# Kernel optimization log

Measured on AMD Instinct MI355X. Metric: run time of the kernel, lower is better.

## Reference

```python
import jax, jax.numpy as jnp
import numpy as np

B, S, D, E, TOPK = 8, 4096, 1024, 64, 2
TEMP = 0.01


def setup_inputs() -> dict:
    key = jax.random.key(0)
    k_x, k_w1, k_b1, k_w2, k_b2 = jax.random.split(key, 5)
    x = jax.random.normal(k_x, (B, S, D), dtype=jnp.float32)
    # torch.nn.Linear default init ~ U(-1/sqrt(fan_in), 1/sqrt(fan_in)); scale ok for reference
    W1 = jax.random.normal(k_w1, (D, 2 * D), dtype=jnp.float32) * (1.0 / np.sqrt(D))
    b1 = jax.random.normal(k_b1, (2 * D,), dtype=jnp.float32) * 0.01
    W2 = jax.random.normal(k_w2, (2 * D, E), dtype=jnp.float32) * (1.0 / np.sqrt(2 * D))
    b2 = jax.random.normal(k_b2, (E,), dtype=jnp.float32) * 0.01
    return {"x": x, "W1": W1, "b1": b1, "W2": W2, "b2": b2}


def reference(x, W1, b1, W2, b2):
    # 2-layer MLP router: [B,S,D] -> [B,S,2D] -> [B,S,E]
    h = jax.nn.relu(jnp.einsum('bsd,df->bsf', x, W1) + b1)
    logits = jnp.einsum('bsf,fe->bse', h, W2) + b2
    # top-k over experts
    top_k_logits, indices = jax.lax.top_k(logits, TOPK)  # [B,S,K]
    # scatter top-k logits into a -inf-filled tensor: equivalent to masking,
    # since scattered values equal logits at those positions
    keep = jax.nn.one_hot(indices, E, dtype=bool).any(axis=-2)  # [B,S,E]
    sparse_logits = jnp.where(keep, logits, -jnp.inf)
    router_output = jax.nn.softmax(sparse_logits, axis=-1)
    ori_router_output = jax.nn.softmax(logits / TEMP, axis=-1)
    return (ori_router_output, router_output, indices)
```

## Files before the change

### kernel.cpp

```cpp
#include <hip/hip_runtime.h>
#include <math.h>
#include <stdint.h>

#define M_TOK 32768
#define D_IN  1024
#define F_HID 2048
#define E_EXP 64

#define O_ORI 0
#define O_RTR (M_TOK * E_EXP)
#define O_IDX (2 * M_TOK * E_EXP)

typedef _Float16 half8 __attribute__((ext_vector_type(8)));
typedef float    f32x4 __attribute__((ext_vector_type(4)));
typedef unsigned int uint32;
typedef uint32   u32x4 __attribute__((ext_vector_type(4)));

#define WS_XH  ((size_t)0)
#define WS_XL  (WS_XH  + (size_t)M_TOK * D_IN * 2)
#define WS_W1H (WS_XL  + (size_t)M_TOK * D_IN * 2)
#define WS_W1L (WS_W1H + (size_t)D_IN * F_HID * 2)
#define WS_W2H (WS_W1L + (size_t)D_IN * F_HID * 2)
#define WS_W2L (WS_W2H + (size_t)F_HID * E_EXP * 2)
#define WS_NEED (WS_W2L + (size_t)F_HID * E_EXP * 2)

__device__ __forceinline__ void split_sc(float v, float sc, unsigned short& h, unsigned short& l) {
    const _Float16 hh = (_Float16)v;
    const float hf = (float)hh;
    const _Float16 hs = (_Float16)(hf * sc);
    const _Float16 ls = (_Float16)((v - hf) * sc);
    h = __builtin_bit_cast(unsigned short, hs);
    l = __builtin_bit_cast(unsigned short, ls);
}


__global__ void split_x_k(const float* __restrict__ x,
                          unsigned short* __restrict__ xh, unsigned short* __restrict__ xl) {
    size_t i = ((size_t)blockIdx.x * 256 + threadIdx.x) * 4;
    const float4 v = *(const float4*)&x[i];
    ushort4 h, l;
    split_sc(v.x, 64.f, h.x, l.x); split_sc(v.y, 64.f, h.y, l.y);
    split_sc(v.z, 64.f, h.z, l.z); split_sc(v.w, 64.f, h.w, l.w);
    *(ushort4*)&xh[i] = h;
    *(ushort4*)&xl[i] = l;
}

__global__ void split_w1t_k(const float* __restrict__ W1,
                            unsigned short* __restrict__ wh, unsigned short* __restrict__ wl) {
    __shared__ float t[32][33];
    const int d0 = blockIdx.x * 32;
    const int f0 = blockIdx.y * 32;
    const int r  = threadIdx.x >> 3;
    const int c4 = (threadIdx.x & 7) * 4;
    const float4 v = *(const float4*)&W1[(size_t)(d0 + r) * F_HID + f0 + c4];
    t[r][c4 + 0] = v.x; t[r][c4 + 1] = v.y; t[r][c4 + 2] = v.z; t[r][c4 + 3] = v.w;
    __syncthreads();
    ushort4 h, l;
    split_sc(t[c4 + 0][r], 64.f, h.x, l.x);
    split_sc(t[c4 + 1][r], 64.f, h.y, l.y);
    split_sc(t[c4 + 2][r], 64.f, h.z, l.z);
    split_sc(t[c4 + 3][r], 64.f, h.w, l.w);
    *(ushort4*)&wh[(size_t)(f0 + r) * D_IN + d0 + c4] = h;
    *(ushort4*)&wl[(size_t)(f0 + r) * D_IN + d0 + c4] = l;
}

__global__ void split_w2f_k(const float* __restrict__ W2,
                            unsigned short* __restrict__ wh, unsigned short* __restrict__ wl) {
    const int s  = blockIdx.x;
    const int nt = threadIdx.x >> 6;
    const int l  = threadIdx.x & 63;
    const int fb = s * 32 + (l >> 4) * 8;
    const int e  = nt * 16 + (l & 15);
    unsigned short h[8], lo[8];
#pragma unroll
    for (int j = 0; j < 8; ++j)
        split_sc(W2[(size_t)(fb + j) * E_EXP + e], 16.f, h[j], lo[j]);
    const size_t base = ((size_t)(s * 4 + nt) * 64 + l) * 8;
    ((ushort4*)&wh[base])[0] = make_ushort4(h[0], h[1], h[2], h[3]);
    ((ushort4*)&wh[base])[1] = make_ushort4(h[4], h[5], h[6], h[7]);
    ((ushort4*)&wl[base])[0] = make_ushort4(lo[0], lo[1], lo[2], lo[3]);
    ((ushort4*)&wl[base])[1] = make_ushort4(lo[4], lo[5], lo[6], lo[7]);
}


__device__ __forceinline__ uint32 swz(uint32 o) { return o ^ (((o >> 7) & 7u) << 4); }

#define STAGE16(SRCP, DSTP) \
    __builtin_amdgcn_global_load_lds((const __attribute__((address_space(1))) void*)(SRCP), \
                                     (__attribute__((address_space(3))) void*)(DSTP), 16, 0, 0)


#define A_BUF(b)  ((b) * 16384)
#define B_BUF(b)  (49152 + (b) * 32768)

__launch_bounds__(512, 2)
__global__ void router_one(const unsigned short* __restrict__ xh, const unsigned short* __restrict__ xl,
                           const unsigned short* __restrict__ w1h, const unsigned short* __restrict__ w1l,
                           const unsigned short* __restrict__ w2fh, const unsigned short* __restrict__ w2fl,
                           const float* __restrict__ b1, const float* __restrict__ b2,
                           float* __restrict__ out)
{
    __shared__ __align__(16) unsigned char lds[147456];

    const int tid  = threadIdx.x;
    const int lane = tid & 63;
    const int w    = tid >> 6;
    const int c15  = lane & 15;
    const int g    = lane >> 4;
    const int wr   = w >> 2;
    const int wc   = w & 3;

    const size_t tok0 = (size_t)blockIdx.x * 128;

    uint32 arow, ahalf, brow[2], bhalf[2];
    {
        const uint32 sA = swz((uint32)(tid * 16));
        arow = sA >> 6; ahalf = (sA & 63u) >> 1;
#pragma unroll
        for (int j = 0; j < 2; ++j) {
            const uint32 sB = swz((uint32)(j * 8192 + w * 1024 + lane * 16));
            brow[j] = sB >> 6; bhalf[j] = (sB & 63u) >> 1;
        }
    }

    uint32 offA[4], offB[4];
#pragma unroll
    for (int m = 0; m < 4; ++m)
        offA[m] = swz((uint32)((wr * 64 + m * 16 + c15) * 64 + g * 16));
#pragma unroll
    for (int n = 0; n < 4; ++n)
        offB[n] = swz((uint32)((wc * 64 + n * 16 + c15) * 64 + g * 16));

    f32x4 acc2[4];
#pragma unroll
    for (int nt = 0; nt < 4; ++nt) acc2[nt] = (f32x4){0.f, 0.f, 0.f, 0.f};

#define STAGE_A(T, WB, F0) do {                                                      \
    const int d0_ = (T) * 32;                                                        \
    const size_t asrc = (tok0 + arow) * D_IN + (size_t)(d0_ + (int)ahalf);           \
    STAGE16(xh + asrc, lds + A_BUF(WB) + w * 1024);                                  \
    STAGE16(xl + asrc, lds + A_BUF(WB) + 8192 + w * 1024);                           \
} while (0)
#define STAGE_B(T, WB, F0, J) do {                                                   \
    const int d0_ = (T) * 32;                                                        \
    const size_t bsrc = ((size_t)(F0) + brow[J]) * D_IN + (size_t)(d0_ + (int)bhalf[J]); \
    STAGE16(w1h + bsrc, lds + B_BUF(WB) + (J) * 8192 + w * 1024);                    \
    STAGE16(w1l + bsrc, lds + B_BUF(WB) + 16384 + (J) * 8192 + w * 1024);            \
} while (0)

#pragma unroll 1
    for (int fc = 0; fc < F_HID; fc += 256) {
        f32x4 acc[4][4];
#pragma unroll
        for (int m = 0; m < 4; ++m)
#pragma unroll
            for (int n = 0; n < 4; ++n) acc[m][n] = (f32x4){0.f, 0.f, 0.f, 0.f};

        __syncthreads();
        STAGE_A(0, 0, fc); STAGE_B(0, 0, fc, 0); STAGE_B(0, 0, fc, 1);
        STAGE_A(1, 1, fc); STAGE_B(1, 1, fc, 0); STAGE_B(1, 1, fc, 1);

#pragma unroll 1
        for (int t = 0; t < 32; ++t) {
            if (t < 31) asm volatile("s_waitcnt vmcnt(6)" ::: "memory");
            else        asm volatile("s_waitcnt vmcnt(0)" ::: "memory");
            __builtin_amdgcn_s_barrier();
            const int rb = t % 3;
            const int wb = (t + 2) % 3;
            const bool do_stage = (t + 2 < 32);
            const unsigned char* Ab = lds + A_BUF(rb);
            const unsigned char* Bb = lds + B_BUF(rb);

            half8 a1f[4], a2f[4], b1f[4], b2f[4];

#pragma unroll
            for (int m = 0; m < 4; ++m) {
                a1f[m] = *(const half8*)(Ab + offA[m]);
                a2f[m] = *(const half8*)(Ab + 8192 + offA[m]);
            }
            b1f[0] = *(const half8*)(Bb + offB[0]);
            b2f[0] = *(const half8*)(Bb + 16384 + offB[0]);
            if (do_stage) STAGE_A(t + 2, wb, fc);
            __builtin_amdgcn_s_barrier();
            asm volatile("s_waitcnt lgkmcnt(0)" ::: "memory");
            __builtin_amdgcn_s_setprio(1);
#pragma unroll
            for (int m = 0; m < 4; ++m) {
                acc[m][0] = __builtin_amdgcn_mfma_f32_16x16x32_f16(a1f[m], b1f[0], acc[m][0], 0, 0, 0);
                acc[m][0] = __builtin_amdgcn_mfma_f32_16x16x32_f16(a1f[m], b2f[0], acc[m][0], 0, 0, 0);
                acc[m][0] = __builtin_amdgcn_mfma_f32_16x16x32_f16(a2f[m], b1f[0], acc[m][0], 0, 0, 0);
            }
            __builtin_amdgcn_s_setprio(0);
            __builtin_amdgcn_s_barrier();

            b1f[1] = *(const half8*)(Bb + offB[1]);
            b2f[1] = *(const half8*)(Bb + 16384 + offB[1]);
            if (do_stage) STAGE_B(t + 2, wb, fc, 0);
            __builtin_amdgcn_s_barrier();
            asm volatile("s_waitcnt lgkmcnt(0)" ::: "memory");
            __builtin_amdgcn_s_setprio(1);
#pragma unroll
            for (int m = 0; m < 4; ++m) {
                acc[m][1] = __builtin_amdgcn_mfma_f32_16x16x32_f16(a1f[m], b1f[1], acc[m][1], 0, 0, 0);
                acc[m][1] = __builtin_amdgcn_mfma_f32_16x16x32_f16(a1f[m], b2f[1], acc[m][1], 0, 0, 0);
                acc[m][1] = __builtin_amdgcn_mfma_f32_16x16x32_f16(a2f[m], b1f[1], acc[m][1], 0, 0, 0);
            }
            __builtin_amdgcn_s_setprio(0);
            __builtin_amdgcn_s_barrier();

            b1f[2] = *(const half8*)(Bb + offB[2]);
            b2f[2] = *(const half8*)(Bb + 16384 + offB[2]);
            if (do_stage) STAGE_B(t + 2, wb, fc, 1);
            __builtin_amdgcn_s_barrier();
            asm volatile("s_waitcnt lgkmcnt(0)" ::: "memory");
            __builtin_amdgcn_s_setprio(1);
#pragma unroll
            for (int m = 0; m < 4; ++m) {
                acc[m][2] = __builtin_amdgcn_mfma_f32_16x16x32_f16(a1f[m], b1f[2], acc[m][2], 0, 0, 0);
                acc[m][2] = __builtin_amdgcn_mfma_f32_16x16x32_f16(a1f[m], b2f[2], acc[m][2], 0, 0, 0);
                acc[m][2] = __builtin_amdgcn_mfma_f32_16x16x32_f16(a2f[m], b1f[2], acc[m][2], 0, 0, 0);
            }
            __builtin_amdgcn_s_setprio(0);
            __builtin_amdgcn_s_barrier();

            b1f[3] = *(const half8*)(Bb + offB[3]);
            b2f[3] = *(const half8*)(Bb + 16384 + offB[3]);
            __builtin_amdgcn_s_barrier();
            asm volatile("s_waitcnt lgkmcnt(0)" ::: "memory");
            __builtin_amdgcn_s_setprio(1);
#pragma unroll
            for (int m = 0; m < 4; ++m) {
                acc[m][3] = __builtin_amdgcn_mfma_f32_16x16x32_f16(a1f[m], b1f[3], acc[m][3], 0, 0, 0);
                acc[m][3] = __builtin_amdgcn_mfma_f32_16x16x32_f16(a1f[m], b2f[3], acc[m][3], 0, 0, 0);
                acc[m][3] = __builtin_amdgcn_mfma_f32_16x16x32_f16(a2f[m], b1f[3], acc[m][3], 0, 0, 0);
            }
            __builtin_amdgcn_s_setprio(0);
        }

        __syncthreads();
        {
            float bv[4];
#pragma unroll
            for (int n = 0; n < 4; ++n) bv[n] = b1[fc + wc * 64 + n * 16 + c15];
#pragma unroll
            for (int m = 0; m < 4; ++m)
#pragma unroll
                for (int n = 0; n < 4; ++n)
#pragma unroll
                    for (int r = 0; r < 4; ++r) {
                        float hv = acc[m][n][r] * (1.f / 4096.f) + bv[n];
                        hv = fmaxf(hv, 0.f);
                        const _Float16 hh = (_Float16)hv;
                        const float hf = (float)hh;
                        const _Float16 hsv = (_Float16)(hf * 16.f);
                        const _Float16 lsv = (_Float16)((hv - hf) * 16.f);
                        const uint32 pk = (uint32)__builtin_bit_cast(unsigned short, hsv)
                                        | ((uint32)__builtin_bit_cast(unsigned short, lsv) << 16);
                        const int tok = wr * 64 + m * 16 + g * 4 + r;
                        const int fl  = wc * 64 + n * 16 + c15;
                        *(uint32*)(lds + tok * 1024 + ((fl * 4) ^ ((tok & 15) << 4))) = pk;
                    }
        }
        __syncthreads();

        {
            const int tokA = w * 16 + c15;
#pragma unroll
            for (int s = 0; s < 8; ++s) {
                const int kf = s * 32 + g * 8;
                const int sg = (fc >> 5) + s;
                half8 bf1[4], bf2[4];
#pragma unroll
                for (int nt = 0; nt < 4; ++nt) {
                    const size_t base = ((size_t)(sg * 4 + nt) * 64 + lane) * 8;
                    bf1[nt] = *(const half8*)&w2fh[base];
                    bf2[nt] = *(const half8*)&w2fl[base];
                }
                const u32x4 q0 = *(const u32x4*)(lds + tokA * 1024 + (((kf    ) * 4) ^ (c15 << 4)));
                const u32x4 q1 = *(const u32x4*)(lds + tokA * 1024 + (((kf + 4) * 4) ^ (c15 << 4)));
                u32x4 hi4, lo4;
                hi4[0] = __builtin_amdgcn_perm(q0[1], q0[0], 0x05040100u);
                hi4[1] = __builtin_amdgcn_perm(q0[3], q0[2], 0x05040100u);
                hi4[2] = __builtin_amdgcn_perm(q1[1], q1[0], 0x05040100u);
                hi4[3] = __builtin_amdgcn_perm(q1[3], q1[2], 0x05040100u);
                lo4[0] = __builtin_amdgcn_perm(q0[1], q0[0], 0x07060302u);
                lo4[1] = __builtin_amdgcn_perm(q0[3], q0[2], 0x07060302u);
                lo4[2] = __builtin_amdgcn_perm(q1[1], q1[0], 0x07060302u);
                lo4[3] = __builtin_amdgcn_perm(q1[3], q1[2], 0x07060302u);
                const half8 a1 = __builtin_bit_cast(half8, hi4);
                const half8 a2 = __builtin_bit_cast(half8, lo4);
#pragma unroll
                for (int nt = 0; nt < 4; ++nt) {
                    acc2[nt] = __builtin_amdgcn_mfma_f32_16x16x32_f16(a1, bf1[nt], acc2[nt], 0, 0, 0);
                    acc2[nt] = __builtin_amdgcn_mfma_f32_16x16x32_f16(a1, bf2[nt], acc2[nt], 0, 0, 0);
                    acc2[nt] = __builtin_amdgcn_mfma_f32_16x16x32_f16(a2, bf1[nt], acc2[nt], 0, 0, 0);
                }
            }
        }
    }
#undef STAGE_A
#undef STAGE_B

    __syncthreads();
    float* ls = (float*)lds;
#pragma unroll
    for (int nt = 0; nt < 4; ++nt)
#pragma unroll
        for (int r = 0; r < 4; ++r) {
            const int tl = w * 16 + g * 4 + r;
            ls[tl * 68 + nt * 16 + c15] = acc2[nt][r] * (1.f / 256.f);
        }
    __syncthreads();

    const int e = lane;
    const float be = b2[e];
#pragma unroll 1
    for (int i = 0; i < 16; ++i) {
        const float l = ls[(w * 16 + i) * 68 + e] + be;

        float v = l; int idx = e;
#pragma unroll
        for (int m = 32; m >= 1; m >>= 1) {
            const float ov = __shfl_xor(v, m, 64);
            const int   oi = __shfl_xor(idx, m, 64);
            if (ov > v || (ov == v && oi < idx)) { v = ov; idx = oi; }
        }
        const float m1 = v; const int i1 = idx;

        v = (e == i1) ? -INFINITY : l; idx = e;
#pragma unroll
        for (int m = 32; m >= 1; m >>= 1) {
            const float ov = __shfl_xor(v, m, 64);
            const int   oi = __shfl_xor(idx, m, 64);
            if (ov > v || (ov == v && oi < idx)) { v = ov; idx = oi; }
        }
        const int i2 = idx;

        const float ex = expf((l - m1) * 100.0f);
        float s = ex;
#pragma unroll
        for (int m = 32; m >= 1; m >>= 1) s += __shfl_xor(s, m, 64);
        const float ori = ex / s;

        const float q = (e == i1 || e == i2) ? expf(l - m1) : 0.f;
        float s2 = q;
#pragma unroll
        for (int m = 32; m >= 1; m >>= 1) s2 += __shfl_xor(s2, m, 64);
        const float rtr = q / s2;

        const size_t tok = tok0 + (size_t)w * 16 + i;
        out[O_ORI + tok * E_EXP + e] = ori;
        out[O_RTR + tok * E_EXP + e] = rtr;
        if (e == 0) {
            out[O_IDX + tok * 2 + 0] = (float)i1;
            out[O_IDX + tok * 2 + 1] = (float)i2;
        }
    }
}


#define BT  64
#define NB  256

__launch_bounds__(256, 2)
__global__ void router_mfma(const unsigned short* __restrict__ xh, const unsigned short* __restrict__ xl,
                            const unsigned short* __restrict__ w1h, const unsigned short* __restrict__ w1l,
                            const unsigned short* __restrict__ w2fh, const unsigned short* __restrict__ w2fl,
                            const float* __restrict__ b1, const float* __restrict__ b2,
                            float* __restrict__ out)
{
    __shared__ __align__(16) unsigned char xs_h[BT * 64];
    __shared__ __align__(16) unsigned char xs_l[BT * 64];
    __shared__ __align__(16) unsigned char w1s_h[NB * 64];
    __shared__ __align__(16) unsigned char w1s_l[NB * 64];
    __shared__ __align__(16) unsigned char hsbuf[BT * 132 * 4];

    const int tid  = threadIdx.x;
    const int lane = tid & 63;
    const int w    = tid >> 6;
    const int c15  = lane & 15;
    const int g    = lane >> 4;
    const size_t tok0 = (size_t)blockIdx.x * BT;

    uint32* hs = (uint32*)hsbuf;
    float*  ls = (float*)hsbuf;

    f32x4 acc2h[4], acc2x[4];
#pragma unroll
    for (int nt = 0; nt < 4; ++nt) {
        acc2h[nt] = (f32x4){0.f, 0.f, 0.f, 0.f};
        acc2x[nt] = (f32x4){0.f, 0.f, 0.f, 0.f};
    }

    const uint32 kqb = (uint32)g * 16u;

    for (int fc = 0; fc < F_HID; fc += NB) {
        f32x4 ahh[4][4], axx[4][4];
#pragma unroll
        for (int mt = 0; mt < 4; ++mt)
#pragma unroll
            for (int nt = 0; nt < 4; ++nt) {
                ahh[mt][nt] = (f32x4){0.f, 0.f, 0.f, 0.f};
                axx[mt][nt] = (f32x4){0.f, 0.f, 0.f, 0.f};
            }

        for (int d0 = 0; d0 < D_IN; d0 += 32) {
            __syncthreads();
            {
                uint32 o = (uint32)w * 1024u + (uint32)lane * 16u;
                uint32 s = swz(o);
                uint32 r = s >> 6, hb = (s & 63u) >> 1;
                const unsigned short* sp;
                sp = xh + (tok0 + r) * D_IN + (size_t)(d0 + (int)hb);
                STAGE16(sp, xs_h + (size_t)w * 1024);
                sp = xl + (tok0 + r) * D_IN + (size_t)(d0 + (int)hb);
                STAGE16(sp, xs_l + (size_t)w * 1024);
#pragma unroll
                for (int q = 0; q < 4; ++q) {
                    const uint32 c_ = (uint32)(q * 4 + w);
                    uint32 o2 = c_ * 1024u + (uint32)lane * 16u;
                    uint32 s2 = swz(o2);
                    uint32 r2 = s2 >> 6, hb2 = (s2 & 63u) >> 1;
                    sp = w1h + ((size_t)(fc + (int)r2)) * D_IN + (size_t)(d0 + (int)hb2);
                    STAGE16(sp, w1s_h + (size_t)c_ * 1024);
                    sp = w1l + ((size_t)(fc + (int)r2)) * D_IN + (size_t)(d0 + (int)hb2);
                    STAGE16(sp, w1s_l + (size_t)c_ * 1024);
                }
            }
            __syncthreads();

            half8 ah[4], al[4], bh[4], bl[4];
#pragma unroll
            for (int mt = 0; mt < 4; ++mt) {
                const uint32 off = swz((uint32)(mt * 16 + c15) * 64u + kqb);
                ah[mt] = *(const half8*)(xs_h + off);
                al[mt] = *(const half8*)(xs_l + off);
            }
#pragma unroll
            for (int nt = 0; nt < 4; ++nt) {
                const uint32 row = (uint32)(w * 64 + nt * 16 + c15);
                const uint32 off = swz(row * 64u + kqb);
                bh[nt] = *(const half8*)(w1s_h + off);
                bl[nt] = *(const half8*)(w1s_l + off);
            }
#pragma unroll
            for (int mt = 0; mt < 4; ++mt)
#pragma unroll
                for (int nt = 0; nt < 4; ++nt) {
                    ahh[mt][nt] = __builtin_amdgcn_mfma_f32_16x16x32_f16(ah[mt], bh[nt], ahh[mt][nt], 0, 0, 0);
                    axx[mt][nt] = __builtin_amdgcn_mfma_f32_16x16x32_f16(ah[mt], bl[nt], axx[mt][nt], 0, 0, 0);
                    axx[mt][nt] = __builtin_amdgcn_mfma_f32_16x16x32_f16(al[mt], bh[nt], axx[mt][nt], 0, 0, 0);
                }
        }

        const int fl0 = (w & 1) * 64;
#pragma unroll
        for (int phase = 0; phase < 2; ++phase) {
            if ((w >> 1) == phase) {
#pragma unroll
                for (int nt = 0; nt < 4; ++nt) {
                    const float b1v = b1[fc + w * 64 + nt * 16 + c15];
#pragma unroll
                    for (int mt = 0; mt < 4; ++mt) {
#pragma unroll
                        for (int r = 0; r < 4; ++r) {
                            float hv = (ahh[mt][nt][r] + axx[mt][nt][r]) * (1.f / 4096.f) + b1v;
                            hv = fmaxf(hv, 0.f);
                            const _Float16 hhv0 = (_Float16)hv;
                            const float hf = (float)hhv0;
                            const _Float16 hhv = (_Float16)(hf * 16.f);
                            const _Float16 hlv = (_Float16)((hv - hf) * 16.f);
                            uint32 pk = (uint32)__builtin_bit_cast(unsigned short, hhv)
                                      | ((uint32)__builtin_bit_cast(unsigned short, hlv) << 16);
                            const int t = mt * 16 + g * 4 + r;
                            hs[t * 132 + fl0 + nt * 16 + c15] = pk;
                        }
                    }
                }
            }
            __syncthreads();
            const int tA = w * 16 + c15;
#pragma unroll
            for (int ktl = 0; ktl < 4; ++ktl) {
                const u32x4 q0 = *(const u32x4*)&hs[tA * 132 + ktl * 32 + g * 8];
                const u32x4 q1 = *(const u32x4*)&hs[tA * 132 + ktl * 32 + g * 8 + 4];
                u32x4 hi4, lo4;
                hi4[0] = __builtin_amdgcn_perm(q0[1], q0[0], 0x05040100u);
                hi4[1] = __builtin_amdgcn_perm(q0[3], q0[2], 0x05040100u);
                hi4[2] = __builtin_amdgcn_perm(q1[1], q1[0], 0x05040100u);
                hi4[3] = __builtin_amdgcn_perm(q1[3], q1[2], 0x05040100u);
                lo4[0] = __builtin_amdgcn_perm(q0[1], q0[0], 0x07060302u);
                lo4[1] = __builtin_amdgcn_perm(q0[3], q0[2], 0x07060302u);
                lo4[2] = __builtin_amdgcn_perm(q1[1], q1[0], 0x07060302u);
                lo4[3] = __builtin_amdgcn_perm(q1[3], q1[2], 0x07060302u);
                const half8 a_h = __builtin_bit_cast(half8, hi4);
                const half8 a_l = __builtin_bit_cast(half8, lo4);
                const int sg = (fc >> 5) + phase * 4 + ktl;
#pragma unroll
                for (int nt = 0; nt < 4; ++nt) {
                    const size_t base = ((size_t)(sg * 4 + nt) * 64 + lane) * 8;
                    const half8 b_h = *(const half8*)&w2fh[base];
                    const half8 b_l = *(const half8*)&w2fl[base];
                    acc2h[nt] = __builtin_amdgcn_mfma_f32_16x16x32_f16(a_h, b_h, acc2h[nt], 0, 0, 0);
                    acc2x[nt] = __builtin_amdgcn_mfma_f32_16x16x32_f16(a_h, b_l, acc2x[nt], 0, 0, 0);
                    acc2x[nt] = __builtin_amdgcn_mfma_f32_16x16x32_f16(a_l, b_h, acc2x[nt], 0, 0, 0);
                }
            }
            __syncthreads();
        }
    }

#pragma unroll
    for (int nt = 0; nt < 4; ++nt)
#pragma unroll
        for (int r = 0; r < 4; ++r) {
            const int t = w * 16 + g * 4 + r;
            ls[t * 68 + nt * 16 + c15] = (acc2h[nt][r] + acc2x[nt][r]) * (1.f / 256.f);
        }
    __syncthreads();

    const int e = lane;
    const float be = b2[e];
#pragma unroll 1
    for (int i = 0; i < 16; ++i) {
        const float l = ls[(w * 16 + i) * 68 + e] + be;

        float v = l; int idx = e;
#pragma unroll
        for (int m = 32; m >= 1; m >>= 1) {
            const float ov = __shfl_xor(v, m, 64);
            const int   oi = __shfl_xor(idx, m, 64);
            if (ov > v || (ov == v && oi < idx)) { v = ov; idx = oi; }
        }
        const float m1 = v; const int i1 = idx;

        v = (e == i1) ? -INFINITY : l; idx = e;
#pragma unroll
        for (int m = 32; m >= 1; m >>= 1) {
            const float ov = __shfl_xor(v, m, 64);
            const int   oi = __shfl_xor(idx, m, 64);
            if (ov > v || (ov == v && oi < idx)) { v = ov; idx = oi; }
        }
        const int i2 = idx;

        const float ex = expf((l - m1) * 100.0f);
        float s = ex;
#pragma unroll
        for (int m = 32; m >= 1; m >>= 1) s += __shfl_xor(s, m, 64);
        const float ori = ex / s;

        const float q = (e == i1 || e == i2) ? expf(l - m1) : 0.f;
        float s2 = q;
#pragma unroll
        for (int m = 32; m >= 1; m >>= 1) s2 += __shfl_xor(s2, m, 64);
        const float rtr = q / s2;

        const size_t tok = tok0 + (size_t)w * 16 + i;
        out[O_ORI + tok * E_EXP + e] = ori;
        out[O_RTR + tok * E_EXP + e] = rtr;
        if (e == 0) {
            out[O_IDX + tok * 2 + 0] = (float)i1;
            out[O_IDX + tok * 2 + 1] = (float)i2;
        }
    }
}


extern "C" void kernel_launch(void* const* d_in, const int* in_sizes, int n_in,
                              void* d_out, int out_size, void* d_ws, size_t ws_size,
                              hipStream_t stream) {
    const float* x  = (const float*)d_in[0];
    const float* W1 = (const float*)d_in[1];
    const float* b1 = (const float*)d_in[2];
    const float* W2 = (const float*)d_in[3];
    const float* b2 = (const float*)d_in[4];
    float* out = (float*)d_out;

    unsigned char* ws = (unsigned char*)d_ws;
    unsigned short* xh  = (unsigned short*)(ws + WS_XH);
    unsigned short* xl  = (unsigned short*)(ws + WS_XL);
    unsigned short* w1h = (unsigned short*)(ws + WS_W1H);
    unsigned short* w1l = (unsigned short*)(ws + WS_W1L);
    unsigned short* w2h = (unsigned short*)(ws + WS_W2H);
    unsigned short* w2l = (unsigned short*)(ws + WS_W2L);

    hipLaunchKernelGGL(split_x_k,  dim3(M_TOK * D_IN / 4 / 256), dim3(256), 0, stream, x, xh, xl);
    hipLaunchKernelGGL(split_w1t_k, dim3(D_IN / 32, F_HID / 32), dim3(256), 0, stream, W1, w1h, w1l);
    hipLaunchKernelGGL(split_w2f_k, dim3(F_HID / 32), dim3(256), 0, stream, W2, w2h, w2l);

    if (ws_size >= WS_NEED) {
        hipLaunchKernelGGL(router_one, dim3(M_TOK / 128), dim3(512), 0, stream,
                           xh, xl, w1h, w1l, w2h, w2l, b1, b2, out);
    } else {
        hipLaunchKernelGGL(router_mfma, dim3(M_TOK / BT), dim3(256), 0, stream,
                           xh, xl, w1h, w1l, w2h, w2l, b1, b2, out);
    }
}
```

Baseline: 498.8 us.

## Switch first GEMM to 32x32x16 MFMA tiles with deeper LDS swizzle

Replaces the 16x16x32 MFMA inner product of the first layer with 32x32x16 MFMA instructions, so each wave computes 2x2 tiles of 32x32 instead of 4x4 tiles of 16x16. LDS fragment reads are regrouped to fit the new operand layout, and the swizzle XORs in additional address bits to avoid bank conflicts under the new access pattern. The per-iteration phases drop from four to two, with both B stagings issued together. The epilogue index mapping is updated to the 32x32 accumulator layout. The larger MFMA should cut LDS traffic per flop and the number of barriers, at the cost of coarser interleaving between loads and compute.

```diff
diff --git a/kernel.cpp b/kernel.cpp
--- a/kernel.cpp
+++ b/kernel.cpp
@@ -12,7 +12,8 @@
 #define O_IDX (2 * M_TOK * E_EXP)
 
 typedef _Float16 half8 __attribute__((ext_vector_type(8)));
-typedef float    f32x4 __attribute__((ext_vector_type(4)));
+typedef float    f32x4  __attribute__((ext_vector_type(4)));
+typedef float    f32x16 __attribute__((ext_vector_type(16)));
 typedef unsigned int uint32;
 typedef uint32   u32x4 __attribute__((ext_vector_type(4)));
 
@@ -83,7 +84,9 @@
 }
 
 
-__device__ __forceinline__ uint32 swz(uint32 o) { return o ^ (((o >> 7) & 7u) << 4); }
+__device__ __forceinline__ uint32 swz(uint32 o) {
+    return o ^ (((((o >> 7) & 7u) ^ ((o >> 10) & 7u))) << 4);
+}
 
 #define STAGE16(SRCP, DSTP) \
     __builtin_amdgcn_global_load_lds((const __attribute__((address_space(1))) void*)(SRCP), \
@@ -107,6 +110,8 @@
     const int w    = tid >> 6;
     const int c15  = lane & 15;
     const int g    = lane >> 4;
+    const int c31  = lane & 31;
+    const int g32  = lane >> 5;
     const int wr   = w >> 2;
     const int wc   = w & 3;
 
@@ -123,19 +128,23 @@
         }
     }
 
-    uint32 offA[4], offB[4];
-#pragma unroll
-    for (int m = 0; m < 4; ++m)
-        offA[m] = swz((uint32)((wr * 64 + m * 16 + c15) * 64 + g * 16));
-#pragma unroll
-    for (int n = 0; n < 4; ++n)
-        offB[n] = swz((uint32)((wc * 64 + n * 16 + c15) * 64 + g * 16));
+    uint32 offA[2][2], offB[2][2];
+#pragma unroll
+    for (int mt = 0; mt < 2; ++mt)
+#pragma unroll
+        for (int ks = 0; ks < 2; ++ks)
+            offA[mt][ks] = swz((uint32)((wr * 64 + mt * 32 + c31) * 64 + ks * 32 + g32 * 16));
+#pragma unroll
+    for (int nt = 0; nt < 2; ++nt)
+#pragma unroll
+        for (int ks = 0; ks < 2; ++ks)
+            offB[nt][ks] = swz((uint32)((wc * 64 + nt * 32 + c31) * 64 + ks * 32 + g32 * 16));
 
     f32x4 acc2[4];
 #pragma unroll
     for (int nt = 0; nt < 4; ++nt) acc2[nt] = (f32x4){0.f, 0.f, 0.f, 0.f};
 
-#define STAGE_A(T, WB, F0) do {                                                      \
+#define STAGE_A(T, WB) do {                                                          \
     const int d0_ = (T) * 32;                                                        \
     const size_t asrc = (tok0 + arow) * D_IN + (size_t)(d0_ + (int)ahalf);           \
     STAGE16(xh + asrc, lds + A_BUF(WB) + w * 1024);                                  \
@@ -150,15 +159,17 @@
 
 #pragma unroll 1
     for (int fc = 0; fc < F_HID; fc += 256) {
-        f32x4 acc[4][4];
-#pragma unroll
-        for (int m = 0; m < 4; ++m)
-#pragma unroll
-            for (int n = 0; n < 4; ++n) acc[m][n] = (f32x4){0.f, 0.f, 0.f, 0.f};
+        f32x16 acc[2][2];
+#pragma unroll
+        for (int m = 0; m < 2; ++m)
+#pragma unroll
+            for (int n = 0; n < 2; ++n)
+#pragma unroll
+                for (int q = 0; q < 16; ++q) acc[m][n][q] = 0.f;
 
         __syncthreads();
-        STAGE_A(0, 0, fc); STAGE_B(0, 0, fc, 0); STAGE_B(0, 0, fc, 1);
-        STAGE_A(1, 1, fc); STAGE_B(1, 1, fc, 0); STAGE_B(1, 1, fc, 1);
+        STAGE_A(0, 0); STAGE_B(0, 0, fc, 0); STAGE_B(0, 0, fc, 1);
+        STAGE_A(1, 1); STAGE_B(1, 1, fc, 0); STAGE_B(1, 1, fc, 1);
 
 #pragma unroll 1
         for (int t = 0; t < 32; ++t) {
@@ -171,84 +182,65 @@
             const unsigned char* Ab = lds + A_BUF(rb);
             const unsigned char* Bb = lds + B_BUF(rb);
 
-            half8 a1f[4], a2f[4], b1f[4], b2f[4];
-
-#pragma unroll
-            for (int m = 0; m < 4; ++m) {
-                a1f[m] = *(const half8*)(Ab + offA[m]);
-                a2f[m] = *(const half8*)(Ab + 8192 + offA[m]);
-            }
-            b1f[0] = *(const half8*)(Bb + offB[0]);
-            b2f[0] = *(const half8*)(Bb + 16384 + offB[0]);
-            if (do_stage) STAGE_A(t + 2, wb, fc);
+            half8 a1f[2][2], a2f[2][2], b1f[2], b2f[2];
+
+#pragma unroll
+            for (int mt = 0; mt < 2; ++mt)
+#pragma unroll
+                for (int ks = 0; ks < 2; ++ks) {
+                    a1f[mt][ks] = *(const half8*)(Ab + offA[mt][ks]);
+                    a2f[mt][ks] = *(const half8*)(Ab + 8192 + offA[mt][ks]);
+                }
+#pragma unroll
+            for (int ks = 0; ks < 2; ++ks) {
+                b1f[ks] = *(const half8*)(Bb + offB[0][ks]);
+                b2f[ks] = *(const half8*)(Bb + 16384 + offB[0][ks]);
+            }
+            if (do_stage) STAGE_A(t + 2, wb);
             __builtin_amdgcn_s_barrier();
             asm volatile("s_waitcnt lgkmcnt(0)" ::: "memory");
             __builtin_amdgcn_s_setprio(1);
 #pragma unroll
-            for (int m = 0; m < 4; ++m) {
-                acc[m][0] = __builtin_amdgcn_mfma_f32_16x16x32_f16(a1f[m], b1f[0], acc[m][0], 0, 0, 0);
-                acc[m][0] = __builtin_amdgcn_mfma_f32_16x16x32_f16(a1f[m], b2f[0], acc[m][0], 0, 0, 0);
-                acc[m][0] = __builtin_amdgcn_mfma_f32_16x16x32_f16(a2f[m], b1f[0], acc[m][0], 0, 0, 0);
-            }
+            for (int mt = 0; mt < 2; ++mt)
+#pragma unroll
+                for (int ks = 0; ks < 2; ++ks) {
+                    acc[mt][0] = __builtin_amdgcn_mfma_f32_32x32x16_f16(a1f[mt][ks], b1f[ks], acc[mt][0], 0, 0, 0);
+                    acc[mt][0] = __builtin_amdgcn_mfma_f32_32x32x16_f16(a1f[mt][ks], b2f[ks], acc[mt][0], 0, 0, 0);
+                    acc[mt][0] = __builtin_amdgcn_mfma_f32_32x32x16_f16(a2f[mt][ks], b1f[ks], acc[mt][0], 0, 0, 0);
+                }
             __builtin_amdgcn_s_setprio(0);
             __builtin_amdgcn_s_barrier();
 
-            b1f[1] = *(const half8*)(Bb + offB[1]);
-            b2f[1] = *(const half8*)(Bb + 16384 + offB[1]);
-            if (do_stage) STAGE_B(t + 2, wb, fc, 0);
+#pragma unroll
+            for (int ks = 0; ks < 2; ++ks) {
+                b1f[ks] = *(const half8*)(Bb + offB[1][ks]);
+                b2f[ks] = *(const half8*)(Bb + 16384 + offB[1][ks]);
+            }
+            if (do_stage) { STAGE_B(t + 2, wb, fc, 0); STAGE_B(t + 2, wb, fc, 1); }
             __builtin_amdgcn_s_barrier();
             asm volatile("s_waitcnt lgkmcnt(0)" ::: "memory");
             __builtin_amdgcn_s_setprio(1);
 #pragma unroll
-            for (int m = 0; m < 4; ++m) {
-                acc[m][1] = __builtin_amdgcn_mfma_f32_16x16x32_f16(a1f[m], b1f[1], acc[m][1], 0, 0, 0);
-                acc[m][1] = __builtin_amdgcn_mfma_f32_16x16x32_f16(a1f[m], b2f[1], acc[m][1], 0, 0, 0);
-                acc[m][1] = __builtin_amdgcn_mfma_f32_16x16x32_f16(a2f[m], b1f[1], acc[m][1], 0, 0, 0);
-            }
-            __builtin_amdgcn_s_setprio(0);
-            __builtin_amdgcn_s_barrier();
-
-            b1f[2] = *(const half8*)(Bb + offB[2]);
-            b2f[2] = *(const half8*)(Bb + 16384 + offB[2]);
-            if (do_stage) STAGE_B(t + 2, wb, fc, 1);
-            __builtin_amdgcn_s_barrier();
-            asm volatile("s_waitcnt lgkmcnt(0)" ::: "memory");
-            __builtin_amdgcn_s_setprio(1);
-#pragma unroll
-            for (int m = 0; m < 4; ++m) {
-                acc[m][2] = __builtin_amdgcn_mfma_f32_16x16x32_f16(a1f[m], b1f[2], acc[m][2], 0, 0, 0);
-                acc[m][2] = __builtin_amdgcn_mfma_f32_16x16x32_f16(a1f[m], b2f[2], acc[m][2], 0, 0, 0);
-                acc[m][2] = __builtin_amdgcn_mfma_f32_16x16x32_f16(a2f[m], b1f[2], acc[m][2], 0, 0, 0);
-            }
-            __builtin_amdgcn_s_setprio(0);
-            __builtin_amdgcn_s_barrier();
-
-            b1f[3] = *(const half8*)(Bb + offB[3]);
-            b2f[3] = *(const half8*)(Bb + 16384 + offB[3]);
-            __builtin_amdgcn_s_barrier();
-            asm volatile("s_waitcnt lgkmcnt(0)" ::: "memory");
-            __builtin_amdgcn_s_setprio(1);
-#pragma unroll
-            for (int m = 0; m < 4; ++m) {
-                acc[m][3] = __builtin_amdgcn_mfma_f32_16x16x32_f16(a1f[m], b1f[3], acc[m][3], 0, 0, 0);
-                acc[m][3] = __builtin_amdgcn_mfma_f32_16x16x32_f16(a1f[m], b2f[3], acc[m][3], 0, 0, 0);
-                acc[m][3] = __builtin_amdgcn_mfma_f32_16x16x32_f16(a2f[m], b1f[3], acc[m][3], 0, 0, 0);
-            }
+            for (int mt = 0; mt < 2; ++mt)
+#pragma unroll
+                for (int ks = 0; ks < 2; ++ks) {
+                    acc[mt][1] = __builtin_amdgcn_mfma_f32_32x32x16_f16(a1f[mt][ks], b1f[ks], acc[mt][1], 0, 0, 0);
+                    acc[mt][1] = __builtin_amdgcn_mfma_f32_32x32x16_f16(a1f[mt][ks], b2f[ks], acc[mt][1], 0, 0, 0);
+                    acc[mt][1] = __builtin_amdgcn_mfma_f32_32x32x16_f16(a2f[mt][ks], b1f[ks], acc[mt][1], 0, 0, 0);
+                }
             __builtin_amdgcn_s_setprio(0);
         }
 
         __syncthreads();
         {
-            float bv[4];
-#pragma unroll
-            for (int n = 0; n < 4; ++n) bv[n] = b1[fc + wc * 64 + n * 16 + c15];
-#pragma unroll
-            for (int m = 0; m < 4; ++m)
-#pragma unroll
-                for (int n = 0; n < 4; ++n)
-#pragma unroll
-                    for (int r = 0; r < 4; ++r) {
-                        float hv = acc[m][n][r] * (1.f / 4096.f) + bv[n];
+#pragma unroll
+            for (int mt = 0; mt < 2; ++mt)
+#pragma unroll
+                for (int nt = 0; nt < 2; ++nt) {
+                    const float bv = b1[fc + wc * 64 + nt * 32 + c31];
+#pragma unroll
+                    for (int r = 0; r < 16; ++r) {
+                        float hv = acc[mt][nt][r] * (1.f / 4096.f) + bv;
                         hv = fmaxf(hv, 0.f);
                         const _Float16 hh = (_Float16)hv;
                         const float hf = (float)hh;
@@ -256,10 +248,11 @@
                         const _Float16 lsv = (_Float16)((hv - hf) * 16.f);
                         const uint32 pk = (uint32)__builtin_bit_cast(unsigned short, hsv)
                                         | ((uint32)__builtin_bit_cast(unsigned short, lsv) << 16);
-                        const int tok = wr * 64 + m * 16 + g * 4 + r;
-                        const int fl  = wc * 64 + n * 16 + c15;
+                        const int tok = wr * 64 + mt * 32 + (r & 3) + 8 * (r >> 2) + 4 * g32;
+                        const int fl  = wc * 64 + nt * 32 + c31;
                         *(uint32*)(lds + tok * 1024 + ((fl * 4) ^ ((tok & 15) << 4))) = pk;
                     }
+                }
         }
         __syncthreads();
 
```

Measured after the change: 531.3 us. 1.07x slower.
